# Optimization experiments

Measured on AMD Instinct MI355X. Metric: run time of the kernel, lower is better.

## Reference

```python
import jax, jax.numpy as jnp
import numpy as np

V, C, TCTX, H, L = 32000, 768, 1024, 12, 6
B, T = 2, 1024
D = C // H
EPS = 1e-5


def setup_inputs() -> dict:
    key = jax.random.key(0)
    ks = jax.random.split(key, 12)
    s = lambda k, shape: jax.random.normal(k, shape, jnp.float32) * 0.02
    return {
        "x_indices": jax.random.randint(ks[0], (B, T), 0, V, jnp.int32),
        "tok_emb": s(ks[1], (V, C)),
        "pos_emb": s(ks[2], (TCTX, C)),
        "ln1_g": jnp.ones((L, C)), "ln1_b": jnp.zeros((L, C)),
        "wq": s(ks[3], (L, C, C)), "wk": s(ks[4], (L, C, C)), "wv": s(ks[5], (L, C, C)),
        "wo": s(ks[6], (L, C, C)), "bo": jnp.zeros((L, C)),
        "ln2_g": jnp.ones((L, C)), "ln2_b": jnp.zeros((L, C)),
        "w1": s(ks[7], (L, C, 4 * C)), "b1": jnp.zeros((L, 4 * C)),
        "w2": s(ks[8], (L, 4 * C, C)), "b2": jnp.zeros((L, C)),
        "lnf_g": jnp.ones((C,)), "lnf_b": jnp.zeros((C,)),
        "wp": s(ks[9], (C, V)), "bp": jnp.zeros((V,)),
    }


def _ln(x, g, b):
    m = x.mean(-1, keepdims=True)
    v = ((x - m) ** 2).mean(-1, keepdims=True)
    return (x - m) * jax.lax.rsqrt(v + EPS) * g + b


def _forward(x_indices, tok_emb, pos_emb, ln1_g, ln1_b, wq, wk, wv, wo, bo,
             ln2_g, ln2_b, w1, b1, w2, b2, lnf_g, lnf_b, wp, bp):
    Bv, Tv = x_indices.shape
    x = tok_emb[x_indices] + pos_emb[:Tv]  # [B,T,C]
    mask = jnp.tril(jnp.ones((Tv, Tv), dtype=bool))  # causal

    def block(x, p):
        g1, be1, q_w, k_w, v_w, o_w, o_b, g2, be2, f1, fb1, f2, fb2 = p
        h = _ln(x, g1, be1)
        q = (h @ q_w).reshape(Bv, Tv, H, D)
        k = (h @ k_w).reshape(Bv, Tv, H, D)
        v = (h @ v_w).reshape(Bv, Tv, H, D)
        scores = jnp.einsum('bthd,bshd->bhts', q, k) / jnp.sqrt(jnp.float32(D))
        scores = jnp.where(mask, scores, -jnp.inf)
        a = jax.nn.softmax(scores, axis=-1)
        o = jnp.einsum('bhts,bshd->bthd', a, v).reshape(Bv, Tv, C)
        x = x + o @ o_w + o_b
        h2 = _ln(x, g2, be2)
        x = x + jax.nn.relu(h2 @ f1 + fb1) @ f2 + fb2
        return x, None

    layer_params = (ln1_g, ln1_b, wq, wk, wv, wo, bo, ln2_g, ln2_b, w1, b1, w2, b2)
    x, _ = jax.lax.scan(block, x, layer_params)
    x = _ln(x, lnf_g, lnf_b)
    return x @ wp + bp  # logits [B,T,V]


def reference(x_indices, tok_emb, pos_emb, ln1_g, ln1_b, wq, wk, wv, wo, bo,
              ln2_g, ln2_b, w1, b1, w2, b2, lnf_g, lnf_b, wp, bp):
    return _forward(x_indices, tok_emb, pos_emb, ln1_g, ln1_b, wq, wk, wv, wo, bo,
                    ln2_g, ln2_b, w1, b1, w2, b2, lnf_g, lnf_b, wp, bp)
```

## Files before the change

### kernel.cpp

```cpp
#include <hip/hip_runtime.h>
#include <stdint.h>

#define DEV __device__ __forceinline__

typedef unsigned short u16;
typedef __attribute__((ext_vector_type(8))) short short8;
typedef __attribute__((ext_vector_type(4))) float floatx4;

#define B_ 2
#define T_ 1024
#define C_ 768
#define H_ 12
#define L_ 6
#define V_ 32000
#define F_ 3072
#define M_ 2048
#define C3_ 2304

#define VMW(n) asm volatile("s_waitcnt vmcnt(" #n ")" ::: "memory")
#define SBAR __builtin_amdgcn_s_barrier()
#define SCHED0 __builtin_amdgcn_sched_barrier(0)

DEV u16 f2bf(float f) {
  unsigned int u; __builtin_memcpy(&u, &f, 4);
  u += 0x7FFFu + ((u >> 16) & 1u);
  return (u16)(u >> 16);
}

DEV void gload16(const void* g, void* l) {
  __builtin_amdgcn_global_load_lds(
      (__attribute__((address_space(1))) void*)(uintptr_t)g,
      (__attribute__((address_space(3))) void*)(unsigned int)(uintptr_t)l,
      16, 0, 0);
}

DEV int xcd_swz(int flat, int nwg) {
  int q = nwg >> 3, r = nwg & 7;
  int xcd = flat & 7, sid = flat >> 3;
  return (xcd < r ? xcd * (q + 1) : r * (q + 1) + (xcd - r) * q) + sid;
}

__global__ __launch_bounds__(256) void transpose_f32_bf16(
    const float* __restrict__ src, u16* __restrict__ dst, int R, int Cc,
    size_t src_z, size_t dst_z) {
  __shared__ float tile[32][33];
  const float* s = src + (size_t)blockIdx.z * src_z;
  u16* d = dst + (size_t)blockIdx.z * dst_z;
  int c0 = blockIdx.x * 32, r0 = blockIdx.y * 32;
  int tx = threadIdx.x & 31, ty = threadIdx.x >> 5;
#pragma unroll
  for (int i = 0; i < 4; i++)
    tile[ty + 8 * i][tx] = s[(size_t)(r0 + ty + 8 * i) * Cc + (c0 + tx)];
  __syncthreads();
#pragma unroll
  for (int i = 0; i < 4; i++)
    d[(size_t)(c0 + ty + 8 * i) * R + (r0 + tx)] = f2bf(tile[tx][ty + 8 * i]);
}

__global__ __launch_bounds__(256) void embed_kernel(
    const int* __restrict__ idx, const float* __restrict__ tok,
    const float* __restrict__ pos, float* __restrict__ x) {
  int row = blockIdx.x;
  int t = row & (T_ - 1);
  int tk = idx[row];
  const float* tp = tok + (size_t)tk * C_;
  const float* pp = pos + (size_t)t * C_;
  float* xp = x + (size_t)row * C_;
  for (int c = threadIdx.x; c < C_; c += 256) xp[c] = tp[c] + pp[c];
}

__global__ __launch_bounds__(256) void ln_kernel(
    const float* __restrict__ x, const float* __restrict__ g,
    const float* __restrict__ b, u16* __restrict__ out) {
  int row = blockIdx.x;
  int tid = threadIdx.x;
  const float* xp = x + (size_t)row * C_;
  float v0 = xp[tid], v1 = xp[tid + 256], v2 = xp[tid + 512];
  float s = v0 + v1 + v2;
  float ss = v0 * v0 + v1 * v1 + v2 * v2;
#pragma unroll
  for (int o = 32; o > 0; o >>= 1) { s += __shfl_down(s, o); ss += __shfl_down(ss, o); }
  __shared__ float red[8];
  int wid = tid >> 6;
  if ((tid & 63) == 0) { red[wid] = s; red[4 + wid] = ss; }
  __syncthreads();
  float tot = red[0] + red[1] + red[2] + red[3];
  float tss = red[4] + red[5] + red[6] + red[7];
  float mean = tot * (1.f / C_);
  float var = tss * (1.f / C_) - mean * mean;
  float rstd = rsqrtf(var + 1e-5f);
  u16* op = out + (size_t)row * C_;
  op[tid]       = f2bf((v0 - mean) * rstd * g[tid]       + b[tid]);
  op[tid + 256] = f2bf((v1 - mean) * rstd * g[tid + 256] + b[tid + 256]);
  op[tid + 512] = f2bf((v2 - mean) * rstd * g[tid + 512] + b[tid + 512]);
}

template <int THREADS, int BM, int BN, int WM, int WN, int BIAS, int RELU, int OUTMODE, int SPLITK>
__global__ __launch_bounds__(THREADS) void gemm3(
    const u16* __restrict__ A, const u16* __restrict__ BT,
    const float* __restrict__ bias,
    u16* __restrict__ ob, float* __restrict__ fout, u16* __restrict__ vt,
    int N, int K) {
  constexpr int ALOADS = (BM * 64) / (THREADS * 16);
  constexpr int BLOADS = (BN * 64) / (THREADS * 16);
  constexpr int LDS_L = ALOADS + BLOADS;
  constexpr int MF = BM / (WM * 16);
  constexpr int NF = BN / (WN * 16);
  __shared__ __align__(16) u16 As[3][BM * 32];
  __shared__ __align__(16) u16 Bs[3][BN * 32];

  int tid = threadIdx.x;
  int lane = tid & 63, w = tid >> 6;
  int wm = w / WN, wn = w % WN;
  int rr = lane & 15, qg = lane >> 4;

  int gx = gridDim.x;
  int nwg = gx * gridDim.y;
  int flat = blockIdx.y * gx + blockIdx.x;
  int wg = xcd_swz(flat, nwg);
  int m0 = (wg % gx) * BM, n0 = (wg / gx) * BN;

  int kz = SPLITK > 1 ? blockIdx.z : 0;
  int Keff = SPLITK > 1 ? (K / SPLITK) : K;
  int kbase = kz * Keff;

  const u16* Aps[ALOADS];
  const u16* Bps[BLOADS];
#pragma unroll
  for (int i = 0; i < ALOADS; i++) {
    int idx = i * THREADS + tid;
    int row = idx >> 2;
    int chunk = (idx & 3) ^ ((row >> 1) & 3);
    Aps[i] = A + (size_t)(m0 + row) * K + chunk * 8 + kbase;
  }
#pragma unroll
  for (int i = 0; i < BLOADS; i++) {
    int idx = i * THREADS + tid;
    int row = idx >> 2;
    int chunk = (idx & 3) ^ ((row >> 1) & 3);
    Bps[i] = BT + (size_t)(n0 + row) * K + chunk * 8 + kbase;
  }

  auto stage = [&](int sl, int kk) {
#pragma unroll
    for (int i = 0; i < ALOADS; i++)
      gload16(Aps[i] + kk, (char*)As + (size_t)sl * BM * 64 + i * THREADS * 16 + w * 1024);
#pragma unroll
    for (int i = 0; i < BLOADS; i++)
      gload16(Bps[i] + kk, (char*)Bs + (size_t)sl * BN * 64 + i * THREADS * 16 + w * 1024);
  };

  floatx4 zero = {0.f, 0.f, 0.f, 0.f};
  floatx4 acc[MF][NF];
#pragma unroll
  for (int i = 0; i < MF; i++)
#pragma unroll
    for (int j = 0; j < NF; j++) acc[i][j] = zero;

  int NT = Keff >> 5;
  stage(0, 0);
  stage(1, 32);
  if constexpr (LDS_L == 2) VMW(2);
  else if constexpr (LDS_L == 3) VMW(3);
  else if constexpr (LDS_L == 4) VMW(4);
  else VMW(6);
  SBAR;
  SCHED0;

  int sqA = (qg ^ ((rr >> 1) & 3)) << 4;

  for (int t = 0; t < NT; ++t) {
    int sl = t % 3;
    if (t + 2 < NT) stage((t + 2) % 3, (t + 2) << 5);
    SCHED0;
    const char* Ab = (const char*)As + (size_t)sl * BM * 64;
    const char* Bb = (const char*)Bs + (size_t)sl * BN * 64;
    short8 af[MF], bf[NF];
#pragma unroll
    for (int i = 0; i < MF; i++)
      af[i] = *(const short8*)(Ab + ((wm * (BM / WM) + i * 16 + rr) << 6) + sqA);
#pragma unroll
    for (int j = 0; j < NF; j++)
      bf[j] = *(const short8*)(Bb + ((wn * (BN / WN) + j * 16 + rr) << 6) + sqA);
    __builtin_amdgcn_s_setprio(1);
#pragma unroll
    for (int i = 0; i < MF; i++)
#pragma unroll
      for (int j = 0; j < NF; j++)
        acc[i][j] = __builtin_amdgcn_mfma_f32_16x16x32_bf16(af[i], bf[j], acc[i][j], 0, 0, 0);
    __builtin_amdgcn_s_setprio(0);
    if (t < NT - 2) {
      if constexpr (LDS_L == 2) VMW(2);
      else if constexpr (LDS_L == 3) VMW(3);
      else if constexpr (LDS_L == 4) VMW(4);
      else VMW(6);
    } else if (t == NT - 2) VMW(0);
    if (t < NT - 1) { SBAR; SCHED0; }
  }

  int cb = n0 + wn * (BN / WN);
  int rb = m0 + wm * (BM / WM);
  bool isv = (OUTMODE == 3) && (n0 >= 1536);
#pragma unroll
  for (int i = 0; i < MF; i++) {
#pragma unroll
    for (int j = 0; j < NF; j++) {
      int col = cb + j * 16 + rr;
      float bv = 0.f;
      if (BIAS && kz == 0) bv = bias[col];
      float vals[4];
#pragma unroll
      for (int r = 0; r < 4; r++) {
        float val = acc[i][j][r] + bv;
        if (RELU) val = fmaxf(val, 0.f);
        vals[r] = val;
      }
      int row0 = rb + i * 16 + qg * 4;
      if (isv) {
        int colv = col - 1536;
        int bb = row0 >> 10, t0 = row0 & (T_ - 1);
        uint2 pk;
        pk.x = (unsigned int)f2bf(vals[0]) | ((unsigned int)f2bf(vals[1]) << 16);
        pk.y = (unsigned int)f2bf(vals[2]) | ((unsigned int)f2bf(vals[3]) << 16);
        *(uint2*)&vt[((size_t)bb * C_ + colv) * T_ + t0] = pk;
      } else {
#pragma unroll
        for (int r = 0; r < 4; r++) {
          size_t o = (size_t)(row0 + r) * N + col;
          if (OUTMODE == 0 || OUTMODE == 3) ob[o] = f2bf(vals[r]);
          else if (OUTMODE == 1) {
            if (SPLITK > 1) atomicAdd(&fout[o], vals[r]);
            else fout[o] += vals[r];
          } else fout[o] = vals[r];
        }
      }
    }
  }
}

__global__ __launch_bounds__(64) void attn_kernel(
    const u16* __restrict__ qkv, const u16* __restrict__ vt, u16* __restrict__ o) {
  __shared__ __align__(16) u16 P_s[16 * 48];
  int nwg = gridDim.x;
  int wg = xcd_swz(blockIdx.x, nwg);
  int qt = wg & 63;
  int h = (wg >> 6) % H_;
  int b = wg / (64 * H_);
  int q0 = qt << 4;
  int lane = threadIdx.x;
  int rr = lane & 15, qg = lane >> 4, kq = qg << 3;

  const u16* qb = qkv + (size_t)(b * T_ + q0 + rr) * C3_ + h * 64;
  short8 qf0 = *(const short8*)(qb + kq);
  short8 qf1 = *(const short8*)(qb + 32 + kq);

  float m_r = -1e30f, l_r = 0.f;
  floatx4 zero = {0.f, 0.f, 0.f, 0.f};
  floatx4 oacc[4];
#pragma unroll
  for (int d = 0; d < 4; d++) oacc[d] = zero;

  const u16* kbase = qkv + (size_t)(b * T_) * C3_ + 768 + h * 64;
  const u16* vbase = vt + (size_t)(b * C_ + h * 64) * T_;

  for (int kt0 = 0; kt0 <= q0 + 15; kt0 += 32) {
    floatx4 s[2];
#pragma unroll
    for (int c = 0; c < 2; c++) {
      const u16* kb = kbase + (size_t)(kt0 + c * 16 + rr) * C3_;
      short8 kf0 = *(const short8*)(kb + kq);
      short8 kf1 = *(const short8*)(kb + 32 + kq);
      floatx4 z = zero;
      z = __builtin_amdgcn_mfma_f32_16x16x32_bf16(kf0, qf0, z, 0, 0, 0);
      z = __builtin_amdgcn_mfma_f32_16x16x32_bf16(kf1, qf1, z, 0, 0, 0);
      s[c] = z;
    }
    int qpos = q0 + rr;
    float p[2][4];
    float mx = -1e30f;
#pragma unroll
    for (int c = 0; c < 2; c++)
#pragma unroll
      for (int r = 0; r < 4; r++) {
        int kpos = kt0 + c * 16 + qg * 4 + r;
        float val = s[c][r] * 0.125f;
        val = (kpos <= qpos) ? val : -1e30f;
        p[c][r] = val;
        mx = fmaxf(mx, val);
      }
    mx = fmaxf(mx, __shfl_xor(mx, 16));
    mx = fmaxf(mx, __shfl_xor(mx, 32));
    float mn = fmaxf(m_r, mx);
    float escL = exp2f((m_r - mn) * 1.44269504f);
    m_r = mn;
    float ps = 0.f;
#pragma unroll
    for (int c = 0; c < 2; c++)
#pragma unroll
      for (int r = 0; r < 4; r++) {
        float pv = exp2f((p[c][r] - mn) * 1.44269504f);
        p[c][r] = pv;
        ps += pv;
      }
    ps += __shfl_xor(ps, 16);
    ps += __shfl_xor(ps, 32);
    l_r = l_r * escL + ps;
#pragma unroll
    for (int c = 0; c < 2; c++) {
      unsigned int u0 = (unsigned int)f2bf(p[c][0]) | ((unsigned int)f2bf(p[c][1]) << 16);
      unsigned int u1 = (unsigned int)f2bf(p[c][2]) | ((unsigned int)f2bf(p[c][3]) << 16);
      uint2 pk; pk.x = u0; pk.y = u1;
      *(uint2*)&P_s[rr * 48 + c * 16 + qg * 4] = pk;
    }
    float er[4];
#pragma unroll
    for (int r = 0; r < 4; r++) er[r] = __shfl(escL, qg * 4 + r);
#pragma unroll
    for (int d = 0; d < 4; d++)
#pragma unroll
      for (int r = 0; r < 4; r++) oacc[d][r] *= er[r];
    short8 pa = *(const short8*)&P_s[rr * 48 + kq];
#pragma unroll
    for (int d = 0; d < 4; d++) {
      short8 vf = *(const short8*)(vbase + (size_t)(d * 16 + rr) * T_ + kt0 + kq);
      oacc[d] = __builtin_amdgcn_mfma_f32_16x16x32_bf16(pa, vf, oacc[d], 0, 0, 0);
    }
  }
  float lb[4];
#pragma unroll
  for (int r = 0; r < 4; r++) lb[r] = __shfl(l_r, qg * 4 + r);
  u16* obp = o + (size_t)(b * T_ + q0) * C_ + h * 64;
#pragma unroll
  for (int d = 0; d < 4; d++)
#pragma unroll
    for (int r = 0; r < 4; r++) {
      int row = qg * 4 + r;
      obp[(size_t)row * C_ + d * 16 + rr] = f2bf(oacc[d][r] / lb[r]);
    }
}

extern "C" void kernel_launch(void* const* d_in, const int* in_sizes, int n_in,
                              void* d_out, int out_size, void* d_ws, size_t ws_size,
                              hipStream_t stream) {
  (void)in_sizes; (void)n_in; (void)out_size; (void)ws_size;
  const int*   xidx = (const int*)d_in[0];
  const float* tok  = (const float*)d_in[1];
  const float* pos  = (const float*)d_in[2];
  const float* ln1g = (const float*)d_in[3];
  const float* ln1b = (const float*)d_in[4];
  const float* wq   = (const float*)d_in[5];
  const float* wk   = (const float*)d_in[6];
  const float* wv   = (const float*)d_in[7];
  const float* wo   = (const float*)d_in[8];
  const float* bo   = (const float*)d_in[9];
  const float* ln2g = (const float*)d_in[10];
  const float* ln2b = (const float*)d_in[11];
  const float* w1   = (const float*)d_in[12];
  const float* b1   = (const float*)d_in[13];
  const float* w2   = (const float*)d_in[14];
  const float* b2   = (const float*)d_in[15];
  const float* lnfg = (const float*)d_in[16];
  const float* lnfb = (const float*)d_in[17];
  const float* wp   = (const float*)d_in[18];
  const float* bp   = (const float*)d_in[19];

  char* ws = (char*)d_ws;
  size_t off = 0;
  auto alloc = [&](size_t bytes) { char* p = ws + off; off += (bytes + 255) & ~(size_t)255; return p; };
  u16* wqkvT = (u16*)alloc((size_t)L_ * 3 * C_ * C_ * 2);
  u16* woT = (u16*)alloc((size_t)L_ * C_ * C_ * 2);
  u16* w1T = (u16*)alloc((size_t)L_ * C_ * F_ * 2);
  u16* w2T = (u16*)alloc((size_t)L_ * C_ * F_ * 2);
  u16* wpT = (u16*)alloc((size_t)C_ * V_ * 2);
  float* x = (float*)alloc((size_t)M_ * C_ * 4);
  u16* hb   = (u16*)alloc((size_t)M_ * C_ * 2);
  u16* qkvb = (u16*)alloc((size_t)M_ * C3_ * 2);
  u16* vtb  = (u16*)alloc((size_t)M_ * C_ * 2);
  u16* aob  = (u16*)alloc((size_t)M_ * C_ * 2);
  u16* mb   = (u16*)alloc((size_t)M_ * F_ * 2);

  dim3 blk(256);
  size_t CC = (size_t)C_ * C_, CF = (size_t)C_ * F_;
  transpose_f32_bf16<<<dim3(C_ / 32, C_ / 32, L_), blk, 0, stream>>>(wq, wqkvT,          C_, C_, CC, 3 * CC);
  transpose_f32_bf16<<<dim3(C_ / 32, C_ / 32, L_), blk, 0, stream>>>(wk, wqkvT + CC,     C_, C_, CC, 3 * CC);
  transpose_f32_bf16<<<dim3(C_ / 32, C_ / 32, L_), blk, 0, stream>>>(wv, wqkvT + 2 * CC, C_, C_, CC, 3 * CC);
  transpose_f32_bf16<<<dim3(C_ / 32, C_ / 32, L_), blk, 0, stream>>>(wo, woT, C_, C_, CC, CC);
  transpose_f32_bf16<<<dim3(F_ / 32, C_ / 32, L_), blk, 0, stream>>>(w1, w1T, C_, F_, CF, CF);
  transpose_f32_bf16<<<dim3(C_ / 32, F_ / 32, L_), blk, 0, stream>>>(w2, w2T, F_, C_, CF, CF);
  transpose_f32_bf16<<<dim3(V_ / 32, C_ / 32, 1), blk, 0, stream>>>(wp, wpT, C_, V_, 0, 0);
  embed_kernel<<<M_, blk, 0, stream>>>(xidx, tok, pos, x);

  for (int l = 0; l < L_; ++l) {
    size_t wOff = (size_t)l * 3 * CC;
    size_t oOff = (size_t)l * CC;
    size_t fOff = (size_t)l * CF;
    ln_kernel<<<M_, blk, 0, stream>>>(x, ln1g + l * C_, ln1b + l * C_, hb);
    gemm3<256, 128, 128, 2, 2, 0, 0, 3, 1><<<dim3(M_ / 128, C3_ / 128), 256, 0, stream>>>(
        hb, wqkvT + wOff, nullptr, qkvb, nullptr, vtb, C3_, C_);
    attn_kernel<<<B_ * H_ * (T_ / 16), dim3(64), 0, stream>>>(qkvb, vtb, aob);
    gemm3<256, 128, 128, 2, 2, 1, 0, 1, 2><<<dim3(M_ / 128, C_ / 128, 2), 256, 0, stream>>>(
        aob, woT + oOff, bo + l * C_, nullptr, x, nullptr, C_, C_);
    ln_kernel<<<M_, blk, 0, stream>>>(x, ln2g + l * C_, ln2b + l * C_, hb);
    gemm3<256, 128, 128, 2, 2, 1, 1, 0, 1><<<dim3(M_ / 128, F_ / 128), 256, 0, stream>>>(
        hb, w1T + fOff, b1 + l * F_, mb, nullptr, nullptr, F_, C_);
    gemm3<256, 128, 128, 2, 2, 1, 0, 1, 2><<<dim3(M_ / 128, C_ / 128, 2), 256, 0, stream>>>(
        mb, w2T + fOff, b2 + l * C_, nullptr, x, nullptr, C_, F_);
  }
  ln_kernel<<<M_, blk, 0, stream>>>(x, lnfg, lnfb, hb);
  gemm3<512, 256, 128, 4, 2, 1, 0, 2, 1><<<dim3(M_ / 256, V_ / 128), 512, 0, stream>>>(
      hb, wpT, bp, nullptr, (float*)d_out, nullptr, V_, C_);
}
```

Before: 1.071 ms.

## Add 256x256 eight-wave pipelined GEMM kernel for the vocabulary projection

```diff
diff --git a/kernel.cpp b/kernel.cpp
--- a/kernel.cpp
+++ b/kernel.cpp
@@ -18,6 +18,7 @@
 #define C3_ 2304
 
 #define VMW(n) asm volatile("s_waitcnt vmcnt(" #n ")" ::: "memory")
+#define LGKM0 asm volatile("s_waitcnt lgkmcnt(0)" ::: "memory")
 #define SBAR __builtin_amdgcn_s_barrier()
 #define SCHED0 __builtin_amdgcn_sched_barrier(0)
 
@@ -234,6 +235,129 @@
           } else fout[o] = vals[r];
         }
       }
+    }
+  }
+}
+
+__global__ __launch_bounds__(512) void gemm8(
+    const u16* __restrict__ A, const u16* __restrict__ BT,
+    const float* __restrict__ bias, float* __restrict__ fout, int N, int K) {
+  __shared__ __align__(16) u16 As[2][2][128 * 64];
+  __shared__ __align__(16) u16 Bs[2][2][128 * 64];
+  int tid = threadIdx.x;
+  int lane = tid & 63, w = tid >> 6;
+  int wr = w >> 2, wc = w & 3;
+  int rr = lane & 15, qg = lane >> 4;
+
+  int gx = gridDim.x;
+  int nwg = gx * gridDim.y;
+  int flat = blockIdx.y * gx + blockIdx.x;
+  int wg = xcd_swz(flat, nwg);
+  int m0 = (wg % gx) * 256, n0 = (wg / gx) * 256;
+
+  int la = tid >> 3;
+  int sa = (((tid & 7) ^ (la & 7)) << 3);
+  const u16* Ap0 = A + (size_t)(m0 + la) * K + sa;
+  const u16* Ap1 = A + (size_t)(m0 + 128 + la) * K + sa;
+  int lb0 = la, lb1 = 64 + la;
+  const u16* Bp0 = BT + (size_t)(n0 + (lb0 >> 5) * 64 + (lb0 & 31)) * K + sa;
+  const u16* Bp1 = BT + (size_t)(n0 + (lb1 >> 5) * 64 + (lb1 & 31)) * K + sa;
+
+  auto stA = [&](int buf, int mh, int kt) {
+    size_t off = (size_t)mh * 64 * K + kt * 64;
+    gload16(Ap0 + off, (char*)&As[buf][mh][0] + w * 1024);
+    gload16(Ap1 + off, (char*)&As[buf][mh][0] + 8192 + w * 1024);
+  };
+  auto stB = [&](int buf, int nh, int kt) {
+    size_t off = (size_t)nh * 32 * K + kt * 64;
+    gload16(Bp0 + off, (char*)&Bs[buf][nh][0] + w * 1024);
+    gload16(Bp1 + off, (char*)&Bs[buf][nh][0] + 8192 + w * 1024);
+  };
+  auto stageOrd = [&](int buf, int h, int kt) {
+    if (h == 0) stA(buf, 0, kt);
+    else if (h == 1) stB(buf, 0, kt);
+    else if (h == 2) stB(buf, 1, kt);
+    else stA(buf, 1, kt);
+  };
+
+  floatx4 zero = {0.f, 0.f, 0.f, 0.f};
+  floatx4 acc[8][4];
+#pragma unroll
+  for (int i = 0; i < 8; i++)
+#pragma unroll
+    for (int j = 0; j < 4; j++) acc[i][j] = zero;
+
+  short8 a[2][4], b[2][2];
+  int NKT = K >> 6;
+  int NIT = NKT >> 1;
+
+  stageOrd(0, 0, 0); stageOrd(0, 1, 0); stageOrd(0, 2, 0); stageOrd(0, 3, 0);
+  VMW(4);
+  SBAR;
+  SCHED0;
+
+  for (int it = 0; it < NIT; ++it) {
+    int kt2 = it * 2;
+    bool last = (it == NIT - 1);
+#pragma unroll
+    for (int p = 0; p < 8; ++p) {
+      const int d = p >> 2;
+      const int q = p & 3;
+      const int mh = q >> 1, nh = q & 1;
+      const char* Abp = (const char*)&As[d][mh][0];
+      const char* Bbp = (const char*)&Bs[d][nh][0];
+      if (q == 0 || q == 2) {
+#pragma unroll
+        for (int kk = 0; kk < 2; kk++)
+#pragma unroll
+          for (int i = 0; i < 4; i++) {
+            int l = wr * 64 + i * 16 + rr;
+            a[kk][i] = *(const short8*)(Abp + l * 128 + ((((kk << 2) + qg) ^ (rr & 7)) << 4));
+          }
+      }
+#pragma unroll
+      for (int kk = 0; kk < 2; kk++)
+#pragma unroll
+        for (int j = 0; j < 2; j++) {
+          int l = wc * 32 + j * 16 + rr;
+          b[kk][j] = *(const short8*)(Bbp + l * 128 + ((((kk << 2) + qg) ^ (rr & 7)) << 4));
+        }
+      if (p < 4) stageOrd(1, q, kt2 + 1);
+      else if (!last) stageOrd(0, q, kt2 + 2);
+      SCHED0;
+      SBAR;
+      LGKM0;
+      SCHED0;
+      __builtin_amdgcn_s_setprio(1);
+#pragma unroll
+      for (int kk = 0; kk < 2; kk++)
+#pragma unroll
+        for (int i = 0; i < 4; i++)
+#pragma unroll
+          for (int j = 0; j < 2; j++)
+            acc[mh * 4 + i][nh * 2 + j] = __builtin_amdgcn_mfma_f32_16x16x32_bf16(
+                a[kk][i], b[kk][j], acc[mh * 4 + i][nh * 2 + j], 0, 0, 0);
+      __builtin_amdgcn_s_setprio(0);
+      if (!last || p < 4) VMW(4);
+      else if (p == 4) VMW(2);
+      else if (p == 5) VMW(0);
+      SBAR;
+      SCHED0;
+    }
+  }
+
+  int rbase = m0 + wr * 128;
+  int cbase = n0 + wc * 64;
+#pragma unroll
+  for (int fi = 0; fi < 8; fi++) {
+    int row0 = rbase + (fi >> 2) * 64 + (fi & 3) * 16 + qg * 4;
+#pragma unroll
+    for (int fj = 0; fj < 4; fj++) {
+      int col = cbase + (fj >> 1) * 32 + (fj & 1) * 16 + rr;
+      float bv = bias[col];
+#pragma unroll
+      for (int r = 0; r < 4; r++)
+        fout[(size_t)(row0 + r) * N + col] = acc[fi][fj][r] + bv;
     }
   }
 }
@@ -407,6 +531,6 @@
         mb, w2T + fOff, b2 + l * C_, nullptr, x, nullptr, C_, F_);
   }
   ln_kernel<<<M_, blk, 0, stream>>>(x, lnfg, lnfb, hb);
-  gemm3<512, 256, 128, 4, 2, 1, 0, 2, 1><<<dim3(M_ / 256, V_ / 128), 512, 0, stream>>>(
-      hb, wpT, bp, nullptr, (float*)d_out, nullptr, V_, C_);
-}
+  gemm8<<<dim3(M_ / 256, V_ / 256), 512, 0, stream>>>(
+      hb, wpT, bp, (float*)d_out, V_, C_);
+}
```

New measurement: 1.066 ms. Within noise of the previous version (-0.5%).
